# Kernel optimization log

Measured on AMD Instinct MI355X. Metric: run time of the kernel, lower is better.

## Reference

```python
import jax, jax.numpy as jnp
import numpy as np

E = 8        # num_experts
D_IN = 512   # num_inputs
H = 256      # num_neurons_expert
T = 64       # num_neurons_tower
B = 16384    # batch


def setup_inputs() -> dict:
    key = jax.random.key(0)
    ks = jax.random.split(key, 7)
    s_in = 1.0 / np.sqrt(D_IN)
    s_h = 1.0 / np.sqrt(H)
    return {
        "xv": jax.random.normal(ks[0], (B, D_IN), dtype=jnp.float32),
        # expert weights stacked: torch Linear weight is (out,in) -> (E, H, D_IN)
        "We": jax.random.uniform(ks[1], (E, H, D_IN), jnp.float32, -s_in, s_in),
        "be": jax.random.uniform(ks[2], (E, H), jnp.float32, -s_in, s_in),
        "Wg": jax.random.uniform(ks[3], (E, D_IN), jnp.float32, -s_in, s_in),
        "bg": jax.random.uniform(ks[4], (E,), jnp.float32, -s_in, s_in),
        "Wt": jax.random.uniform(ks[5], (T, H), jnp.float32, -s_h, s_h),
        "bt": jax.random.uniform(ks[6], (T,), jnp.float32, -s_h, s_h),
    }


def reference(xv, We, be, Wg, bg, Wt, bt):
    # All experts as one batched GEMM: [B,D] x [E,H,D] -> [B,E,H]
    experts = jax.nn.relu(jnp.einsum("bd,ehd->beh", xv, We) + be[None, :, :])
    # Dropout is identity in eval mode.
    gate = jax.nn.softmax(xv @ Wg.T + bg, axis=1)            # [B,E]
    combined = jnp.einsum("beh,be->bh", experts, gate)        # [B,H]
    out = jax.nn.sigmoid(combined @ Wt.T + bt)                # [B,T]
    return out
```

## Files before the change

kernel.cpp:

```cpp
#include <hip/hip_runtime.h>
#include <hip/hip_bf16.h>
#include <stdint.h>

typedef unsigned short u16;
typedef __bf16 bf16x8 __attribute__((ext_vector_type(8)));
typedef float f32x4 __attribute__((ext_vector_type(4)));

#define LDS_A_USH 8192
#define LDS_B_USH 16384

__device__ __forceinline__ void glds16(const void* g, void* l) {
  __builtin_amdgcn_global_load_lds(
      (const __attribute__((address_space(1))) unsigned int*)g,
      (__attribute__((address_space(3))) unsigned int*)l, 16, 0, 0);
}

__device__ __forceinline__ u16 f2bf(float f) {
  unsigned int u = __builtin_bit_cast(unsigned int, f);
  u += 0x7fffu + ((u >> 16) & 1u);
  return (u16)(u >> 16);
}

__global__ __launch_bounds__(256) void prep_kernel(
    const float* __restrict__ xv, const float* __restrict__ We,
    const float* __restrict__ Wg, const float* __restrict__ bg,
    const float* __restrict__ Wt,
    u16* __restrict__ xv_bf, u16* __restrict__ We_bf,
    u16* __restrict__ Wt_bf, float* __restrict__ gate) {
  const int bx = blockIdx.x;
  if (bx < 4096) {
    const int wid = threadIdx.x >> 6, lane = threadIdx.x & 63;
    const int row = bx * 4 + wid;
    const float* xr = xv + (row << 9) + lane * 8;
    float4 x0 = *(const float4*)xr;
    float4 x1 = *(const float4*)(xr + 4);
    uint4 o;
    o.x = (unsigned)f2bf(x0.x) | ((unsigned)f2bf(x0.y) << 16);
    o.y = (unsigned)f2bf(x0.z) | ((unsigned)f2bf(x0.w) << 16);
    o.z = (unsigned)f2bf(x1.x) | ((unsigned)f2bf(x1.y) << 16);
    o.w = (unsigned)f2bf(x1.z) | ((unsigned)f2bf(x1.w) << 16);
    *(uint4*)(xv_bf + (row << 9) + lane * 8) = o;
    float s[8];
#pragma unroll
    for (int e = 0; e < 8; e++) {
      const float* wg = Wg + (e << 9) + lane * 8;
      float4 w0 = *(const float4*)wg;
      float4 w1 = *(const float4*)(wg + 4);
      s[e] = x0.x * w0.x + x0.y * w0.y + x0.z * w0.z + x0.w * w0.w +
             x1.x * w1.x + x1.y * w1.y + x1.z * w1.z + x1.w * w1.w;
    }
#pragma unroll
    for (int e = 0; e < 8; e++) {
#pragma unroll
      for (int off = 32; off > 0; off >>= 1) s[e] += __shfl_xor(s[e], off);
      s[e] += bg[e];
    }
    float mx = s[0];
#pragma unroll
    for (int e = 1; e < 8; e++) mx = fmaxf(mx, s[e]);
    float p[8], sum = 0.f;
#pragma unroll
    for (int e = 0; e < 8; e++) { p[e] = __expf(s[e] - mx); sum += p[e]; }
    float inv = 1.f / sum;
    if (lane == 0) {
      float4 g0 = {p[0] * inv, p[1] * inv, p[2] * inv, p[3] * inv};
      float4 g1 = {p[4] * inv, p[5] * inv, p[6] * inv, p[7] * inv};
      *(float4*)(gate + row * 8) = g0;
      *(float4*)(gate + row * 8 + 4) = g1;
    }
  } else {
    const int base = (bx - 4096) * 2048 + threadIdx.x * 8;
    const float* src;
    u16* dst;
    if (base < 1048576) { src = We + base; dst = We_bf + base; }
    else { src = Wt + (base - 1048576); dst = Wt_bf + (base - 1048576); }
    float4 a = *(const float4*)src;
    float4 b = *(const float4*)(src + 4);
    uint4 o;
    o.x = (unsigned)f2bf(a.x) | ((unsigned)f2bf(a.y) << 16);
    o.y = (unsigned)f2bf(a.z) | ((unsigned)f2bf(a.w) << 16);
    o.z = (unsigned)f2bf(b.x) | ((unsigned)f2bf(b.y) << 16);
    o.w = (unsigned)f2bf(b.z) | ((unsigned)f2bf(b.w) << 16);
    *(uint4*)dst = o;
  }
}

__global__ __launch_bounds__(256, 2) void moe_main(
    const u16* __restrict__ xv_bf, const u16* __restrict__ We_bf,
    const float* __restrict__ be, const float* __restrict__ gate,
    const u16* __restrict__ Wt_bf, float* __restrict__ part) {
  __shared__ u16 lds[LDS_A_USH + LDS_B_USH];

  const int bx = blockIdx.x;
  const int mb = bx >> 1;
  const int hb = bx & 1;
  const int m0 = mb << 6;
  const int tid = threadIdx.x;
  const int lane = tid & 63;
  const int wid = tid >> 6;
  const int wm = wid >> 1;
  const int wn = wid & 1;
  const int l15 = lane & 15;
  const int l4 = lane >> 4;

  f32x4 comb[2][4];
#pragma unroll
  for (int mt = 0; mt < 2; mt++)
#pragma unroll
    for (int nt = 0; nt < 4; nt++) comb[mt][nt] = {0.f, 0.f, 0.f, 0.f};

  for (int e = 0; e < 8; e++) {
    f32x4 acc[2][4];
#pragma unroll
    for (int mt = 0; mt < 2; mt++)
#pragma unroll
      for (int nt = 0; nt < 4; nt++) acc[mt][nt] = {0.f, 0.f, 0.f, 0.f};

    const u16* Wb = We_bf + (e << 17);
    for (int kc = 0; kc < 4; kc++) {
      __syncthreads();
      const int kofs = kc << 7;
#pragma unroll
      for (int r = 0; r < 4; r++) {
        int gi = r * 256 + tid;
        int m = gi >> 4, s = gi & 15;
        int g = (s & 8) | ((s & 7) ^ (m & 7));
        glds16(xv_bf + ((m0 + m) << 9) + kofs + (g << 3), &lds[gi << 3]);
      }
#pragma unroll
      for (int r = 0; r < 8; r++) {
        int gi = r * 256 + tid;
        int n = gi >> 4, s = gi & 15;
        int g = (s & 8) | ((s & 7) ^ (n & 7));
        glds16(Wb + (((hb << 7) + n) << 9) + kofs + (g << 3),
               &lds[LDS_A_USH + (gi << 3)]);
      }
      __syncthreads();
#pragma unroll
      for (int ks = 0; ks < 4; ks++) {
        const int gg = ks * 4 + l4;
        bf16x8 af[2], bfr[4];
#pragma unroll
        for (int mt = 0; mt < 2; mt++) {
          int row = wm * 32 + mt * 16 + l15;
          int slot = (gg & 8) | ((gg & 7) ^ (row & 7));
          af[mt] = *(const bf16x8*)&lds[(row << 7) + (slot << 3)];
        }
#pragma unroll
        for (int nt = 0; nt < 4; nt++) {
          int n = wn * 64 + nt * 16 + l15;
          int slot = (gg & 8) | ((gg & 7) ^ (n & 7));
          bfr[nt] = *(const bf16x8*)&lds[LDS_A_USH + (n << 7) + (slot << 3)];
        }
#pragma unroll
        for (int mt = 0; mt < 2; mt++)
#pragma unroll
          for (int nt = 0; nt < 4; nt++)
            acc[mt][nt] = __builtin_amdgcn_mfma_f32_16x16x32_bf16(
                af[mt], bfr[nt], acc[mt][nt], 0, 0, 0);
      }
    }
    float bev[4];
#pragma unroll
    for (int nt = 0; nt < 4; nt++)
      bev[nt] = be[(e << 8) + (hb << 7) + wn * 64 + nt * 16 + l15];
#pragma unroll
    for (int mt = 0; mt < 2; mt++) {
#pragma unroll
      for (int i = 0; i < 4; i++) {
        float g = gate[((m0 + wm * 32 + mt * 16 + l4 * 4 + i) << 3) + e];
#pragma unroll
        for (int nt = 0; nt < 4; nt++)
          comb[mt][nt][i] += g * fmaxf(acc[mt][nt][i] + bev[nt], 0.f);
      }
    }
  }

  __syncthreads();
#pragma unroll
  for (int mt = 0; mt < 2; mt++)
#pragma unroll
    for (int i = 0; i < 4; i++) {
      int row = wm * 32 + mt * 16 + l4 * 4 + i;
#pragma unroll
      for (int nt = 0; nt < 4; nt++) {
        int col = wn * 64 + nt * 16 + l15;
        __bf16 v = (__bf16)comb[mt][nt][i];
        lds[row * 136 + col] = __builtin_bit_cast(u16, v);
      }
    }
  __syncthreads();
  f32x4 tacc[4];
#pragma unroll
  for (int nt = 0; nt < 4; nt++) tacc[nt] = {0.f, 0.f, 0.f, 0.f};
  const u16* WtB = Wt_bf + (hb << 7);
#pragma unroll
  for (int kc = 0; kc < 4; kc++) {
    int ko = kc * 32 + l4 * 8;
    bf16x8 aT = *(const bf16x8*)&lds[(wid * 16 + l15) * 136 + ko];
#pragma unroll
    for (int nt = 0; nt < 4; nt++) {
      bf16x8 bT = *(const bf16x8*)&WtB[(nt * 16 + l15) * 256 + ko];
      tacc[nt] = __builtin_amdgcn_mfma_f32_16x16x32_bf16(aT, bT, tacc[nt], 0, 0, 0);
    }
  }
  float* pout = part + hb * 1048576;
#pragma unroll
  for (int nt = 0; nt < 4; nt++)
#pragma unroll
    for (int i = 0; i < 4; i++) {
      int grow = m0 + wid * 16 + l4 * 4 + i;
      pout[grow * 64 + nt * 16 + l15] = tacc[nt][i];
    }
}

__global__ __launch_bounds__(256) void finish_kernel(
    const float* __restrict__ part, const float* __restrict__ bt,
    float* __restrict__ out) {
  const int idx = (blockIdx.x * 256 + threadIdx.x) << 2;
  float4 a = *(const float4*)(part + idx);
  float4 b = *(const float4*)(part + 1048576 + idx);
  float4 c = *(const float4*)(bt + (idx & 63));
  float4 r;
  r.x = 1.f / (1.f + __expf(-(a.x + b.x + c.x)));
  r.y = 1.f / (1.f + __expf(-(a.y + b.y + c.y)));
  r.z = 1.f / (1.f + __expf(-(a.z + b.z + c.z)));
  r.w = 1.f / (1.f + __expf(-(a.w + b.w + c.w)));
  *(float4*)(out + idx) = r;
}

extern "C" void kernel_launch(void* const* d_in, const int* in_sizes, int n_in,
                              void* d_out, int out_size, void* d_ws, size_t ws_size,
                              hipStream_t stream) {
  const float* xv = (const float*)d_in[0];
  const float* We = (const float*)d_in[1];
  const float* be = (const float*)d_in[2];
  const float* Wg = (const float*)d_in[3];
  const float* bg = (const float*)d_in[4];
  const float* Wt = (const float*)d_in[5];
  const float* bt = (const float*)d_in[6];

  char* ws = (char*)d_ws;
  u16* xv_bf = (u16*)ws;
  u16* We_bf = (u16*)(ws + 16777216);
  u16* Wt_bf = (u16*)(ws + 18874368);
  float* gate = (float*)(ws + 18907136);
  float* part = (float*)(ws + 19431424);

  prep_kernel<<<4616, 256, 0, stream>>>(xv, We, Wg, bg, Wt, xv_bf, We_bf, Wt_bf, gate);
  moe_main<<<512, 256, 0, stream>>>(xv_bf, We_bf, be, gate, Wt_bf, part);
  finish_kernel<<<1024, 256, 0, stream>>>(part, bt, (float*)d_out);
}
```

Measured before the change: 152.4 us.

## Split MoE work per expert with 32x32 MFMA tiles and bf16 partials

```diff
diff --git a/kernel.cpp b/kernel.cpp
--- a/kernel.cpp
+++ b/kernel.cpp
@@ -1,13 +1,13 @@
 #include <hip/hip_runtime.h>
-#include <hip/hip_bf16.h>
 #include <stdint.h>
 
 typedef unsigned short u16;
 typedef __bf16 bf16x8 __attribute__((ext_vector_type(8)));
 typedef float f32x4 __attribute__((ext_vector_type(4)));
-
-#define LDS_A_USH 8192
-#define LDS_B_USH 16384
+typedef float f32x16 __attribute__((ext_vector_type(16)));
+
+#define XV_N 8388608
+#define WE_N 1048576
 
 __device__ __forceinline__ void glds16(const void* g, void* l) {
   __builtin_amdgcn_global_load_lds(
@@ -19,6 +19,10 @@
   unsigned int u = __builtin_bit_cast(unsigned int, f);
   u += 0x7fffu + ((u >> 16) & 1u);
   return (u16)(u >> 16);
+}
+
+__device__ __forceinline__ float bf2f(u16 u) {
+  return __builtin_bit_cast(float, ((unsigned int)u) << 16);
 }
 
 __global__ __launch_bounds__(256) void prep_kernel(
@@ -72,8 +76,8 @@
     const int base = (bx - 4096) * 2048 + threadIdx.x * 8;
     const float* src;
     u16* dst;
-    if (base < 1048576) { src = We + base; dst = We_bf + base; }
-    else { src = Wt + (base - 1048576); dst = Wt_bf + (base - 1048576); }
+    if (base < WE_N) { src = We + base; dst = We_bf + base; }
+    else { src = Wt + (base - WE_N); dst = Wt_bf + (base - WE_N); }
     float4 a = *(const float4*)src;
     float4 b = *(const float4*)(src + 4);
     uint4 o;
@@ -88,145 +92,156 @@
 __global__ __launch_bounds__(256, 2) void moe_main(
     const u16* __restrict__ xv_bf, const u16* __restrict__ We_bf,
     const float* __restrict__ be, const float* __restrict__ gate,
-    const u16* __restrict__ Wt_bf, float* __restrict__ part) {
-  __shared__ u16 lds[LDS_A_USH + LDS_B_USH];
+    const u16* __restrict__ Wt_bf, u16* __restrict__ part) {
+  __shared__ u16 lds[24576];
 
   const int bx = blockIdx.x;
-  const int mb = bx >> 1;
-  const int hb = bx & 1;
-  const int m0 = mb << 6;
-  const int tid = threadIdx.x;
-  const int lane = tid & 63;
-  const int wid = tid >> 6;
-  const int wm = wid >> 1;
-  const int wn = wid & 1;
-  const int l15 = lane & 15;
-  const int l4 = lane >> 4;
-
-  f32x4 comb[2][4];
+  const int e = bx & 7, mb = bx >> 3;
+  const int m0 = mb << 7;
+  const int tid = threadIdx.x, lane = tid & 63, wid = tid >> 6;
+  const int wm = wid >> 1, wn = wid & 1;
+  const int l31 = lane & 31, lhi = lane >> 5;
+  const int l15 = lane & 15, l4 = lane >> 4;
+
+  f32x16 acc[2][4];
 #pragma unroll
   for (int mt = 0; mt < 2; mt++)
 #pragma unroll
-    for (int nt = 0; nt < 4; nt++) comb[mt][nt] = {0.f, 0.f, 0.f, 0.f};
-
-  for (int e = 0; e < 8; e++) {
-    f32x4 acc[2][4];
-#pragma unroll
-    for (int mt = 0; mt < 2; mt++)
-#pragma unroll
-      for (int nt = 0; nt < 4; nt++) acc[mt][nt] = {0.f, 0.f, 0.f, 0.f};
-
-    const u16* Wb = We_bf + (e << 17);
-    for (int kc = 0; kc < 4; kc++) {
-      __syncthreads();
-      const int kofs = kc << 7;
-#pragma unroll
-      for (int r = 0; r < 4; r++) {
-        int gi = r * 256 + tid;
-        int m = gi >> 4, s = gi & 15;
-        int g = (s & 8) | ((s & 7) ^ (m & 7));
-        glds16(xv_bf + ((m0 + m) << 9) + kofs + (g << 3), &lds[gi << 3]);
-      }
-#pragma unroll
-      for (int r = 0; r < 8; r++) {
-        int gi = r * 256 + tid;
-        int n = gi >> 4, s = gi & 15;
-        int g = (s & 8) | ((s & 7) ^ (n & 7));
-        glds16(Wb + (((hb << 7) + n) << 9) + kofs + (g << 3),
-               &lds[LDS_A_USH + (gi << 3)]);
-      }
-      __syncthreads();
-#pragma unroll
-      for (int ks = 0; ks < 4; ks++) {
-        const int gg = ks * 4 + l4;
-        bf16x8 af[2], bfr[4];
-#pragma unroll
-        for (int mt = 0; mt < 2; mt++) {
-          int row = wm * 32 + mt * 16 + l15;
-          int slot = (gg & 8) | ((gg & 7) ^ (row & 7));
-          af[mt] = *(const bf16x8*)&lds[(row << 7) + (slot << 3)];
+    for (int nt = 0; nt < 4; nt++)
+#pragma unroll
+      for (int r = 0; r < 16; r++) acc[mt][nt][r] = 0.f;
+
+  const u16* Wb = We_bf + (e << 17);
+  for (int kc = 0; kc < 8; kc++) {
+    const int kofs = kc << 6;
+    __syncthreads();
+#pragma unroll
+    for (int r = 0; r < 4; r++) {
+      int gi = r * 256 + tid;
+      int m = gi >> 3, s = gi & 7, g = s ^ (m & 7);
+      glds16(xv_bf + ((m0 + m) << 9) + kofs + (g << 3), &lds[gi << 3]);
+    }
+#pragma unroll
+    for (int r = 0; r < 8; r++) {
+      int gi = r * 256 + tid;
+      int n = gi >> 3, s = gi & 7, g = s ^ (n & 7);
+      glds16(Wb + (n << 9) + kofs + (g << 3), &lds[8192 + (gi << 3)]);
+    }
+    __syncthreads();
+#pragma unroll
+    for (int ks = 0; ks < 4; ks++) {
+      const int gg = ks * 2 + lhi;
+      bf16x8 af[2];
+#pragma unroll
+      for (int mt = 0; mt < 2; mt++) {
+        int m = wm * 64 + mt * 32 + l31;
+        int slot = gg ^ (m & 7);
+        af[mt] = *(const bf16x8*)&lds[(m << 6) + (slot << 3)];
+      }
+      bf16x8 bfr[4];
+#pragma unroll
+      for (int nt = 0; nt < 4; nt++) {
+        int n = wn * 128 + nt * 32 + l31;
+        int slot = gg ^ (n & 7);
+        bfr[nt] = *(const bf16x8*)&lds[8192 + (n << 6) + (slot << 3)];
+      }
+#pragma unroll
+      for (int mt = 0; mt < 2; mt++)
+#pragma unroll
+        for (int nt = 0; nt < 4; nt++)
+          acc[mt][nt] = __builtin_amdgcn_mfma_f32_32x32x16_bf16(
+              af[mt], bfr[nt], acc[mt][nt], 0, 0, 0);
+    }
+  }
+
+  float bev[4];
+#pragma unroll
+  for (int nt = 0; nt < 4; nt++)
+    bev[nt] = be[(e << 8) + wn * 128 + nt * 32 + l31];
+
+  f32x4 tacc[2][4];
+#pragma unroll
+  for (int mt = 0; mt < 2; mt++)
+#pragma unroll
+    for (int nt = 0; nt < 4; nt++) tacc[mt][nt] = {0.f, 0.f, 0.f, 0.f};
+
+  __syncthreads();
+
+#pragma unroll
+  for (int half = 0; half < 2; half++) {
+    if (wn == half) {
+#pragma unroll
+      for (int mt = 0; mt < 2; mt++) {
+#pragma unroll
+        for (int r = 0; r < 16; r++) {
+          int rowpat = (r & 3) + 8 * (r >> 2) + 4 * lhi;
+          int row = wm * 64 + mt * 32 + rowpat;
+          float g = gate[((m0 + row) << 3) + e];
+#pragma unroll
+          for (int nt = 0; nt < 4; nt++) {
+            float c = g * fmaxf(acc[mt][nt][r] + bev[nt], 0.f);
+            lds[row * 136 + nt * 32 + l31] = f2bf(c);
+          }
         }
-#pragma unroll
-        for (int nt = 0; nt < 4; nt++) {
-          int n = wn * 64 + nt * 16 + l15;
-          int slot = (gg & 8) | ((gg & 7) ^ (n & 7));
-          bfr[nt] = *(const bf16x8*)&lds[LDS_A_USH + (n << 7) + (slot << 3)];
+      }
+    }
+    __syncthreads();
+#pragma unroll
+    for (int ks = 0; ks < 4; ks++) {
+#pragma unroll
+      for (int mtt = 0; mtt < 2; mtt++) {
+        bf16x8 aT = *(const bf16x8*)&lds[(wid * 32 + mtt * 16 + l15) * 136 +
+                                         ks * 32 + l4 * 8];
+#pragma unroll
+        for (int ntt = 0; ntt < 4; ntt++) {
+          bf16x8 bT = *(const bf16x8*)&Wt_bf[(ntt * 16 + l15) * 256 +
+                                             half * 128 + ks * 32 + l4 * 8];
+          tacc[mtt][ntt] = __builtin_amdgcn_mfma_f32_16x16x32_bf16(
+              aT, bT, tacc[mtt][ntt], 0, 0, 0);
         }
-#pragma unroll
-        for (int mt = 0; mt < 2; mt++)
-#pragma unroll
-          for (int nt = 0; nt < 4; nt++)
-            acc[mt][nt] = __builtin_amdgcn_mfma_f32_16x16x32_bf16(
-                af[mt], bfr[nt], acc[mt][nt], 0, 0, 0);
-      }
-    }
-    float bev[4];
-#pragma unroll
-    for (int nt = 0; nt < 4; nt++)
-      bev[nt] = be[(e << 8) + (hb << 7) + wn * 64 + nt * 16 + l15];
-#pragma unroll
-    for (int mt = 0; mt < 2; mt++) {
+      }
+    }
+    __syncthreads();
+  }
+
+  u16* pout = part + (e << 20);
+#pragma unroll
+  for (int mtt = 0; mtt < 2; mtt++)
+#pragma unroll
+    for (int ntt = 0; ntt < 4; ntt++)
 #pragma unroll
       for (int i = 0; i < 4; i++) {
-        float g = gate[((m0 + wm * 32 + mt * 16 + l4 * 4 + i) << 3) + e];
-#pragma unroll
-        for (int nt = 0; nt < 4; nt++)
-          comb[mt][nt][i] += g * fmaxf(acc[mt][nt][i] + bev[nt], 0.f);
-      }
-    }
-  }
-
-  __syncthreads();
-#pragma unroll
-  for (int mt = 0; mt < 2; mt++)
-#pragma unroll
-    for (int i = 0; i < 4; i++) {
-      int row = wm * 32 + mt * 16 + l4 * 4 + i;
-#pragma unroll
-      for (int nt = 0; nt < 4; nt++) {
-        int col = wn * 64 + nt * 16 + l15;
-        __bf16 v = (__bf16)comb[mt][nt][i];
-        lds[row * 136 + col] = __builtin_bit_cast(u16, v);
-      }
-    }
-  __syncthreads();
-  f32x4 tacc[4];
-#pragma unroll
-  for (int nt = 0; nt < 4; nt++) tacc[nt] = {0.f, 0.f, 0.f, 0.f};
-  const u16* WtB = Wt_bf + (hb << 7);
-#pragma unroll
-  for (int kc = 0; kc < 4; kc++) {
-    int ko = kc * 32 + l4 * 8;
-    bf16x8 aT = *(const bf16x8*)&lds[(wid * 16 + l15) * 136 + ko];
-#pragma unroll
-    for (int nt = 0; nt < 4; nt++) {
-      bf16x8 bT = *(const bf16x8*)&WtB[(nt * 16 + l15) * 256 + ko];
-      tacc[nt] = __builtin_amdgcn_mfma_f32_16x16x32_bf16(aT, bT, tacc[nt], 0, 0, 0);
-    }
-  }
-  float* pout = part + hb * 1048576;
-#pragma unroll
-  for (int nt = 0; nt < 4; nt++)
-#pragma unroll
-    for (int i = 0; i < 4; i++) {
-      int grow = m0 + wid * 16 + l4 * 4 + i;
-      pout[grow * 64 + nt * 16 + l15] = tacc[nt][i];
-    }
+        int grow = m0 + wid * 32 + mtt * 16 + l4 * 4 + i;
+        pout[grow * 64 + ntt * 16 + l15] = f2bf(tacc[mtt][ntt][i]);
+      }
 }
 
 __global__ __launch_bounds__(256) void finish_kernel(
-    const float* __restrict__ part, const float* __restrict__ bt,
+    const u16* __restrict__ part, const float* __restrict__ bt,
     float* __restrict__ out) {
-  const int idx = (blockIdx.x * 256 + threadIdx.x) << 2;
-  float4 a = *(const float4*)(part + idx);
-  float4 b = *(const float4*)(part + 1048576 + idx);
-  float4 c = *(const float4*)(bt + (idx & 63));
-  float4 r;
-  r.x = 1.f / (1.f + __expf(-(a.x + b.x + c.x)));
-  r.y = 1.f / (1.f + __expf(-(a.y + b.y + c.y)));
-  r.z = 1.f / (1.f + __expf(-(a.z + b.z + c.z)));
-  r.w = 1.f / (1.f + __expf(-(a.w + b.w + c.w)));
-  *(float4*)(out + idx) = r;
+  const int base = (blockIdx.x * 256 + threadIdx.x) * 8;
+  float a[8] = {0.f, 0.f, 0.f, 0.f, 0.f, 0.f, 0.f, 0.f};
+#pragma unroll
+  for (int s = 0; s < 8; s++) {
+    uint4 p = *(const uint4*)(part + s * 1048576 + base);
+    a[0] += bf2f((u16)p.x); a[1] += bf2f((u16)(p.x >> 16));
+    a[2] += bf2f((u16)p.y); a[3] += bf2f((u16)(p.y >> 16));
+    a[4] += bf2f((u16)p.z); a[5] += bf2f((u16)(p.z >> 16));
+    a[6] += bf2f((u16)p.w); a[7] += bf2f((u16)(p.w >> 16));
+  }
+  const int t0 = base & 63;
+  float4 b0 = *(const float4*)(bt + t0);
+  float4 b1 = *(const float4*)(bt + t0 + 4);
+  float r[8];
+#pragma unroll
+  for (int j = 0; j < 8; j++) {
+    float bj = (j < 4) ? (&b0.x)[j] : (&b1.x)[j - 4];
+    r[j] = 1.f / (1.f + __expf(-(a[j] + bj)));
+  }
+  float4 o0 = {r[0], r[1], r[2], r[3]};
+  float4 o1 = {r[4], r[5], r[6], r[7]};
+  *(float4*)(out + base) = o0;
+  *(float4*)(out + base + 4) = o1;
 }
 
 extern "C" void kernel_launch(void* const* d_in, const int* in_sizes, int n_in,
@@ -245,9 +260,9 @@
   u16* We_bf = (u16*)(ws + 16777216);
   u16* Wt_bf = (u16*)(ws + 18874368);
   float* gate = (float*)(ws + 18907136);
-  float* part = (float*)(ws + 19431424);
+  u16* part = (u16*)(ws + 19431424);
 
   prep_kernel<<<4616, 256, 0, stream>>>(xv, We, Wg, bg, Wt, xv_bf, We_bf, Wt_bf, gate);
-  moe_main<<<512, 256, 0, stream>>>(xv_bf, We_bf, be, gate, Wt_bf, part);
-  finish_kernel<<<1024, 256, 0, stream>>>(part, bt, (float*)d_out);
-}
+  moe_main<<<1024, 256, 0, stream>>>(xv_bf, We_bf, be, gate, Wt_bf, part);
+  finish_kernel<<<512, 256, 0, stream>>>(part, bt, (float*)d_out);
+}
```

Result: slower. 159.3 us (+4.5%).
